# Kernel optimization log

Hardware: AMD Instinct MI355X
Metric: run time of the kernel (lower is better)

## Reference

```python
import jax, jax.numpy as jnp
import numpy as np

BS, HID, INP, SPAN, OUT, DAYS = 32768, 128, 64, 8, 2, 20


def _init(key, shape, fan_in):
    # mimic torch default uniform(-1/sqrt(fan), 1/sqrt(fan)) init
    bound = 1.0 / np.sqrt(fan_in)
    return jax.random.uniform(key, shape, jnp.float32, -bound, bound)


def setup_inputs() -> dict:
    key = jax.random.key(0)
    ks = jax.random.split(key, 11)
    return {
        "hx": jax.random.normal(ks[0], (BS, HID), jnp.float32),
        # GRUCell params (PyTorch layout: gates stacked [r, z, n])
        "w_ih": _init(ks[1], (3 * HID, INP), HID),
        "w_hh": _init(ks[2], (3 * HID, HID), HID),
        "b_ih": _init(ks[3], (3 * HID,), HID),
        "b_hh": _init(ks[4], (3 * HID,), HID),
        # fc_in: hid -> input
        "fc_in_w": _init(ks[5], (INP, HID), HID),
        "fc_in_b": _init(ks[6], (INP,), HID),
        # fc_out: hid -> out
        "fc_out_w": _init(ks[7], (OUT, HID), HID),
        "fc_out_b": _init(ks[8], (OUT,), HID),
        # num_span_layer: hid -> num_span_classes
        "span_w": _init(ks[9], (SPAN, HID), HID),
        "span_b": _init(ks[10], (SPAN,), HID),
    }


def _gru_cell(x, h, w_ih, w_hh, b_ih, b_hh):
    gi = x @ w_ih.T + b_ih  # [B, 3H]
    gh = h @ w_hh.T + b_hh  # [B, 3H]
    i_r, i_z, i_n = jnp.split(gi, 3, axis=-1)
    h_r, h_z, h_n = jnp.split(gh, 3, axis=-1)
    r = jax.nn.sigmoid(i_r + h_r)
    z = jax.nn.sigmoid(i_z + h_z)
    n = jnp.tanh(i_n + r * h_n)
    return (1.0 - z) * n + z * h


def reference(hx, w_ih, w_hh, b_ih, b_hh, fc_in_w, fc_in_b,
              fc_out_w, fc_out_b, span_w, span_b):
    num_spans = jax.nn.softmax(hx @ span_w.T + span_b, axis=-1)  # [B, SPAN]
    x0 = jnp.zeros((hx.shape[0], fc_in_w.shape[0]), hx.dtype)  # zero first input

    def step(carry, _):
        h, x = carry
        h = _gru_cell(x, h, w_ih, w_hh, b_ih, b_hh)
        x = jax.nn.relu(h @ fc_in_w.T + fc_in_b)
        out = jax.nn.softmax(h @ fc_out_w.T + fc_out_b, axis=-1)  # [B, OUT]
        return (h, x), out

    _, outs = jax.lax.scan(step, (hx, x0), None, length=DAYS)  # [DAYS, B, OUT]
    outputs = jnp.transpose(outs, (1, 0, 2))  # [B, DAYS, OUT]
    return num_spans, outputs
```

## Files before the change

### kernel.cpp

```cpp
#include <hip/hip_runtime.h>
#include <hip/hip_bf16.h>

#define HID 128
#define INP 64
#define SPANN 8
#define NOUT 2
#define DAYS 20
#define RT 4
#define ROWS (16*RT)
#define NTH 512

typedef __attribute__((ext_vector_type(8))) short short8;
typedef __attribute__((ext_vector_type(4))) float f32x4;
typedef __attribute__((ext_vector_type(2))) float f32x2;
typedef unsigned int u32;
typedef __attribute__((ext_vector_type(2))) u32 u32x2;
typedef unsigned short u16;

#define MFMA(a,b,c) __builtin_amdgcn_mfma_f32_16x16x32_bf16(a,b,c,0,0,0)
#define RCPF(x)  __builtin_amdgcn_rcpf(x)
#define EXP2F(x) __builtin_amdgcn_exp2f(x)
#define LOG2E   1.4426950408889634f
#define NLOG2E  (-1.4426950408889634f)
#define LOG2E2  2.8853900817779268f

__device__ __forceinline__ u32 pack2(float a, float b){
    __hip_bfloat162 h = __float22bfloat162_rn(float2{a, b});
    u32 r; __builtin_memcpy(&r, &h, 4); return r;
}
__device__ __forceinline__ float asF(u32 u){ union{u32 u; float f;} v; v.u = u; return v.f; }
__device__ __forceinline__ float sig2(float a){ return RCPF(1.0f + EXP2F(a)); }
__device__ __forceinline__ float tanh2(float a){ return fmaf(-2.0f, RCPF(1.0f + EXP2F(a)), 1.0f); }

union frag_u { short8 s; u32 w[4]; };
__device__ __forceinline__ short8 ldfrag(const float* p, float sc){
    const f32x4 a = *(const f32x4*)p;
    const f32x4 b = *(const f32x4*)(p+4);
    frag_u f;
    f.w[0] = pack2(sc*a[0],sc*a[1]); f.w[1] = pack2(sc*a[2],sc*a[3]);
    f.w[2] = pack2(sc*b[0],sc*b[1]); f.w[3] = pack2(sc*b[2],sc*b[3]);
    return f.s;
}


__global__ __launch_bounds__(NTH, 2) void gru_mfma(
    const float* __restrict__ hx, const float* __restrict__ w_ih,
    const float* __restrict__ w_hh, const float* __restrict__ b_ih,
    const float* __restrict__ b_hh, const float* __restrict__ fc_in_w,
    const float* __restrict__ fc_in_b, const float* __restrict__ fc_out_w,
    const float* __restrict__ fc_out_b, const float* __restrict__ span_w,
    const float* __restrict__ span_b, float* __restrict__ out, int bs)
{
    __shared__ u16 hL[2][RT*2048];
    __shared__ u16 xL[RT*1024];
    __shared__ u16 finL[4*4*64*8];
    __shared__ float diffP[ROWS][9];

    const int tid = threadIdx.x;
    const int wid = tid >> 6;
    const int l   = tid & 63;
    const int r15 = l & 15;
    const int hi  = l >> 4;
    const int row0 = blockIdx.x * ROWS;
    const int mB  = wid & 3;
    const int rtB_off = wid >> 2;

    short8 whhR[4], whhZ[4], whhN[4];
    short8 wihR[2], wihZ[2], wihN[2];
    const int g0 = wid*16 + r15;
    #pragma unroll
    for (int ks = 0; ks < 4; ++ks){
        whhR[ks] = ldfrag(w_hh + (size_t)(      g0)*HID + ks*32 + hi*8, NLOG2E);
        whhZ[ks] = ldfrag(w_hh + (size_t)(128 + g0)*HID + ks*32 + hi*8, NLOG2E);
        whhN[ks] = ldfrag(w_hh + (size_t)(256 + g0)*HID + ks*32 + hi*8, LOG2E2);
    }
    #pragma unroll
    for (int ks = 0; ks < 2; ++ks){
        wihR[ks] = ldfrag(w_ih + (size_t)(      g0)*INP + ks*32 + hi*8, NLOG2E);
        wihZ[ks] = ldfrag(w_ih + (size_t)(128 + g0)*INP + ks*32 + hi*8, NLOG2E);
        wihN[ks] = ldfrag(w_ih + (size_t)(256 + g0)*INP + ks*32 + hi*8, LOG2E2);
    }

    for (int s = tid; s < 1024; s += NTH) {
        const int mt = s >> 8, ks = (s >> 6) & 3, ll = s & 63;
        short8 f = ldfrag(fc_in_w + (size_t)(mt*16 + (ll&15))*HID + ks*32 + (ll>>4)*8, 1.0f);
        *((short8*)finL + s) = f;
    }

    f32x4 bRv, bZv, bNiv, bNhv, fbv, wd4;
    const int c0 = wid*16 + hi*4;
    #pragma unroll
    for (int q = 0; q < 4; ++q){
        const int g = c0 + q;
        bRv[q]  = NLOG2E*(b_ih[g]       + b_hh[g]);
        bZv[q]  = NLOG2E*(b_ih[128 + g] + b_hh[128 + g]);
        bNiv[q] = LOG2E2* b_ih[256 + g];
        bNhv[q] = LOG2E2* b_hh[256 + g];
        fbv[q]  = fc_in_b[mB*16 + hi*4 + q];
        wd4[q]  = NLOG2E*(fc_out_w[g] - fc_out_w[HID + g]);
    }
    const float bd = NLOG2E*(fc_out_b[0] - fc_out_b[1]);

    const int wu32  = (wid>>1)*256 + (((wid&1)*2 + (hi>>1))*16 + r15)*4 + (hi&1)*2;
    const int xwu32 = (mB >>1)*256 + (((mB &1)*2 + (hi>>1))*16 + r15)*4 + (hi&1)*2;

    {
        #pragma unroll
        for (int rt = 0; rt < RT; ++rt){
            const f32x4 h4 = *(const f32x4*)(hx + (size_t)(row0 + rt*16 + r15)*HID + c0);
            u32x2 wv; wv[0] = pack2(h4[0], h4[1]); wv[1] = pack2(h4[2], h4[3]);
            *(u32x2*)((u32*)&hL[0][rt*2048] + wu32) = wv;
        }
        u32* xb = (u32*)&xL[0];
        for (int i = tid; i < RT*512; i += NTH) xb[i] = 0u;
    }
    __syncthreads();

    if (wid < 4){
        const short8 zz = {0,0,0,0,0,0,0,0};
        short8 spw[4];
        #pragma unroll
        for (int ks = 0; ks < 4; ++ks)
            spw[ks] = (r15 < SPANN) ? ldfrag(span_w + (size_t)r15*HID + ks*32 + hi*8, 1.0f) : zz;
        f32x4 acc = {0.f,0.f,0.f,0.f};
        #pragma unroll
        for (int q = 0; q < 4; ++q) if (hi < 2) acc[q] = span_b[hi*4 + q];
        const short8* hf = (const short8*)&hL[0][wid*2048];
        #pragma unroll
        for (int ks = 0; ks < 4; ++ks) acc = MFMA(spw[ks], hf[ks*64 + l], acc);
        if (hi < 2){
            float m = fmaxf(fmaxf(acc[0], acc[1]), fmaxf(acc[2], acc[3]));
            m = fmaxf(m, __shfl_xor(m, 16));
            float e0 = EXP2F(LOG2E*(acc[0]-m)), e1 = EXP2F(LOG2E*(acc[1]-m));
            float e2 = EXP2F(LOG2E*(acc[2]-m)), e3 = EXP2F(LOG2E*(acc[3]-m));
            float s = e0 + e1 + e2 + e3;
            s += __shfl_xor(s, 16);
            const float inv = RCPF(s);
            f32x4 o = {e0*inv, e1*inv, e2*inv, e3*inv};
            *(f32x4*)(out + (size_t)(row0 + wid*16 + r15)*SPANN + hi*4) = o;
        }
    }

    float* __restrict__ outp = out + (size_t)bs * SPANN;

    #define TILE_A(RTG, hRd_, hWr_) do { \
        const short8* hf = (const short8*)((hRd_) + (RTG)*2048); \
        const short8* xf = (const short8*)(xL + (RTG)*1024); \
        const short8 h0=hf[l], h1=hf[64+l], h2=hf[128+l], h3=hf[192+l]; \
        const short8 x0=xf[l], x1=xf[64+l]; \
        const u32x2 ho = *(const u32x2*)((const u32*)(hRd_) + (RTG)*1024 + wu32); \
        f32x4 aR  = MFMA(whhR[0], h0, bRv); \
        f32x4 aZ  = MFMA(whhZ[0], h0, bZv); \
        f32x4 aNh = MFMA(whhN[0], h0, bNhv); \
        aR = MFMA(whhR[1],h1,aR); aZ = MFMA(whhZ[1],h1,aZ); aNh = MFMA(whhN[1],h1,aNh); \
        aR = MFMA(whhR[2],h2,aR); aZ = MFMA(whhZ[2],h2,aZ); aNh = MFMA(whhN[2],h2,aNh); \
        aR = MFMA(whhR[3],h3,aR); aZ = MFMA(whhZ[3],h3,aZ); aNh = MFMA(whhN[3],h3,aNh); \
        f32x4 aNi = MFMA(wihN[0], x0, bNiv); \
        aR = MFMA(wihR[0],x0,aR); aZ = MFMA(wihZ[0],x0,aZ); \
        aNi = MFMA(wihN[1],x1,aNi); \
        aR = MFMA(wihR[1],x1,aR); aZ = MFMA(wihZ[1],x1,aZ); \
        const float hold[4] = { asF(ho[0]<<16), asF(ho[0]&0xFFFF0000u), \
                                asF(ho[1]<<16), asF(ho[1]&0xFFFF0000u) }; \
        float hn[4]; \
        _Pragma("unroll") for (int q=0;q<4;++q){ \
            const float rg = sig2(aR[q]); const float zg = sig2(aZ[q]); \
            const float nn = tanh2(fmaf(rg, aNh[q], aNi[q])); \
            hn[q] = fmaf(zg, hold[q]-nn, nn); } \
        u32x2 wv; wv[0]=pack2(hn[0],hn[1]); wv[1]=pack2(hn[2],hn[3]); \
        *(u32x2*)((hWr_) + (RTG)*1024 + wu32) = wv; \
        float pd = hn[0]*wd4[0]; pd = fmaf(hn[1],wd4[1],pd); \
        pd = fmaf(hn[2],wd4[2],pd); pd = fmaf(hn[3],wd4[3],pd); \
        pd += __shfl_xor(pd, 16); pd += __shfl_xor(pd, 32); \
        if (hi == 0) diffP[(RTG)*16 + r15][wid] = pd; \
    } while(0)

    #define OUT_STORE(d_, gb_) do { \
        if (wid == 7 && l < 32) { \
            const int rowIdx = (gb_)*32 + l; \
            const float* dp = &diffP[rowIdx][0]; \
            const float s = ((dp[0]+dp[1])+(dp[2]+dp[3])) + ((dp[4]+dp[5])+(dp[6]+dp[7])); \
            const float p0 = sig2(s + bd); \
            f32x2 o = {p0, 1.0f - p0}; \
            *(f32x2*)(outp + ((size_t)(row0 + rowIdx)*DAYS + (d_))*NOUT) = o; \
        } \
    } while(0)

    #define TILE_B(d_, gb_, hSrc) do { \
        if ((d_) < DAYS-1) { \
            const int rtB = 2*(gb_) + rtB_off; \
            const short8* hf = (const short8*)((hSrc) + rtB*2048); \
            const short8 h0=hf[l], h1=hf[64+l], h2=hf[128+l], h3=hf[192+l]; \
            const short8* fp = (const short8*)finL + mB*256 + l; \
            f32x4 ax = MFMA(fp[0],   h0, fbv); \
            ax       = MFMA(fp[64],  h1, ax); \
            ax       = MFMA(fp[128], h2, ax); \
            ax       = MFMA(fp[192], h3, ax); \
            u32x2 wv; \
            wv[0] = pack2(fmaxf(ax[0],0.f), fmaxf(ax[1],0.f)); \
            wv[1] = pack2(fmaxf(ax[2],0.f), fmaxf(ax[3],0.f)); \
            *(u32x2*)((u32*)xL + rtB*512 + xwu32) = wv; \
        } \
        OUT_STORE(d_, gb_); \
    } while(0)

    #pragma unroll 1
    for (int d = 0; d < DAYS; ++d){
        const u16* hRd = hL[d & 1];
        u32*       hWr = (u32*)hL[(d & 1) ^ 1];

        TILE_A(0, hRd, hWr);
        TILE_A(1, hRd, hWr);
        if (d > 0) TILE_B(d-1, 1, hRd);
        __syncthreads();

        TILE_A(2, hRd, hWr);
        TILE_A(3, hRd, hWr);
        TILE_B(d, 0, (const u16*)hWr);
        __syncthreads();
    }
    OUT_STORE(DAYS-1, 1);

    #undef TILE_A
    #undef TILE_B
    #undef OUT_STORE
}

extern "C" void kernel_launch(void* const* d_in, const int* in_sizes, int n_in,
                              void* d_out, int out_size, void* d_ws, size_t ws_size,
                              hipStream_t stream) {
    const float* hx       = (const float*)d_in[0];
    const float* w_ih     = (const float*)d_in[1];
    const float* w_hh     = (const float*)d_in[2];
    const float* b_ih     = (const float*)d_in[3];
    const float* b_hh     = (const float*)d_in[4];
    const float* fc_in_w  = (const float*)d_in[5];
    const float* fc_in_b  = (const float*)d_in[6];
    const float* fc_out_w = (const float*)d_in[7];
    const float* fc_out_b = (const float*)d_in[8];
    const float* span_w   = (const float*)d_in[9];
    const float* span_b   = (const float*)d_in[10];
    float* out = (float*)d_out;

    const int bs = in_sizes[0] / HID;
    dim3 grid(bs / ROWS), block(NTH);
    gru_mfma<<<grid, block, 0, stream>>>(hx, w_ih, w_hh, b_ih, b_hh,
                                         fc_in_w, fc_in_b, fc_out_w, fc_out_b,
                                         span_w, span_b, out, bs);
}
```

Before: 143.3 us.

## Stagger GRU and fc_in tile order across waves, keep hidden state in registers

Odd waves now run the fc_in (TILE_B) matmul before their GRU tiles, while even waves keep the original order. This is meant to spread MFMA and LDS pressure between barriers. Each wave also keeps its previous hidden-state slice in fp32 registers instead of re-reading the bf16 copy from LDS, which drops one LDS load per tile and avoids bf16 rounding of the z*h term. MFMA blocks are wrapped in s_setprio, and the diffP reduction now uses padded, aligned vector reads. The cost is more live registers, which could hurt occupancy at two blocks of 512 threads.

```diff
diff --git a/kernel.cpp b/kernel.cpp
--- a/kernel.cpp
+++ b/kernel.cpp
@@ -28,7 +28,6 @@
     __hip_bfloat162 h = __float22bfloat162_rn(float2{a, b});
     u32 r; __builtin_memcpy(&r, &h, 4); return r;
 }
-__device__ __forceinline__ float asF(u32 u){ union{u32 u; float f;} v; v.u = u; return v.f; }
 __device__ __forceinline__ float sig2(float a){ return RCPF(1.0f + EXP2F(a)); }
 __device__ __forceinline__ float tanh2(float a){ return fmaf(-2.0f, RCPF(1.0f + EXP2F(a)), 1.0f); }
 
@@ -54,7 +53,7 @@
     __shared__ u16 hL[2][RT*2048];
     __shared__ u16 xL[RT*1024];
     __shared__ u16 finL[4*4*64*8];
-    __shared__ float diffP[ROWS][9];
+    __shared__ __attribute__((aligned(16))) float diffP[ROWS][12];
 
     const int tid = threadIdx.x;
     const int wid = tid >> 6;
@@ -104,13 +103,15 @@
     const int wu32  = (wid>>1)*256 + (((wid&1)*2 + (hi>>1))*16 + r15)*4 + (hi&1)*2;
     const int xwu32 = (mB >>1)*256 + (((mB &1)*2 + (hi>>1))*16 + r15)*4 + (hi&1)*2;
 
+    f32x4 hOld0, hOld1, hOld2, hOld3;
     {
-        #pragma unroll
-        for (int rt = 0; rt < RT; ++rt){
-            const f32x4 h4 = *(const f32x4*)(hx + (size_t)(row0 + rt*16 + r15)*HID + c0);
-            u32x2 wv; wv[0] = pack2(h4[0], h4[1]); wv[1] = pack2(h4[2], h4[3]);
-            *(u32x2*)((u32*)&hL[0][rt*2048] + wu32) = wv;
-        }
+        #define LOADH(RTG, HO) do { \
+            const f32x4 h4 = *(const f32x4*)(hx + (size_t)(row0 + (RTG)*16 + r15)*HID + c0); \
+            HO = h4; \
+            u32x2 wv; wv[0] = pack2(h4[0], h4[1]); wv[1] = pack2(h4[2], h4[3]); \
+            *(u32x2*)((u32*)&hL[0][(RTG)*2048] + wu32) = wv; } while(0)
+        LOADH(0, hOld0); LOADH(1, hOld1); LOADH(2, hOld2); LOADH(3, hOld3);
+        #undef LOADH
         u32* xb = (u32*)&xL[0];
         for (int i = tid; i < RT*512; i += NTH) xb[i] = 0u;
     }
@@ -143,12 +144,12 @@
 
     float* __restrict__ outp = out + (size_t)bs * SPANN;
 
-    #define TILE_A(RTG, hRd_, hWr_) do { \
+    #define TILE_A(RTG, hRd_, hWr_, HO) do { \
         const short8* hf = (const short8*)((hRd_) + (RTG)*2048); \
         const short8* xf = (const short8*)(xL + (RTG)*1024); \
         const short8 h0=hf[l], h1=hf[64+l], h2=hf[128+l], h3=hf[192+l]; \
         const short8 x0=xf[l], x1=xf[64+l]; \
-        const u32x2 ho = *(const u32x2*)((const u32*)(hRd_) + (RTG)*1024 + wu32); \
+        __builtin_amdgcn_s_setprio(1); \
         f32x4 aR  = MFMA(whhR[0], h0, bRv); \
         f32x4 aZ  = MFMA(whhZ[0], h0, bZv); \
         f32x4 aNh = MFMA(whhN[0], h0, bNhv); \
@@ -159,13 +160,12 @@
         aR = MFMA(wihR[0],x0,aR); aZ = MFMA(wihZ[0],x0,aZ); \
         aNi = MFMA(wihN[1],x1,aNi); \
         aR = MFMA(wihR[1],x1,aR); aZ = MFMA(wihZ[1],x1,aZ); \
-        const float hold[4] = { asF(ho[0]<<16), asF(ho[0]&0xFFFF0000u), \
-                                asF(ho[1]<<16), asF(ho[1]&0xFFFF0000u) }; \
+        __builtin_amdgcn_s_setprio(0); \
         float hn[4]; \
         _Pragma("unroll") for (int q=0;q<4;++q){ \
             const float rg = sig2(aR[q]); const float zg = sig2(aZ[q]); \
             const float nn = tanh2(fmaf(rg, aNh[q], aNi[q])); \
-            hn[q] = fmaf(zg, hold[q]-nn, nn); } \
+            hn[q] = fmaf(zg, HO[q]-nn, nn); HO[q] = hn[q]; } \
         u32x2 wv; wv[0]=pack2(hn[0],hn[1]); wv[1]=pack2(hn[2],hn[3]); \
         *(u32x2*)((hWr_) + (RTG)*1024 + wu32) = wv; \
         float pd = hn[0]*wd4[0]; pd = fmaf(hn[1],wd4[1],pd); \
@@ -177,8 +177,9 @@
     #define OUT_STORE(d_, gb_) do { \
         if (wid == 7 && l < 32) { \
             const int rowIdx = (gb_)*32 + l; \
-            const float* dp = &diffP[rowIdx][0]; \
-            const float s = ((dp[0]+dp[1])+(dp[2]+dp[3])) + ((dp[4]+dp[5])+(dp[6]+dp[7])); \
+            const f32x4 v0 = *(const f32x4*)&diffP[rowIdx][0]; \
+            const f32x4 v1 = *(const f32x4*)&diffP[rowIdx][4]; \
+            const float s = ((v0[0]+v0[1])+(v0[2]+v0[3])) + ((v1[0]+v1[1])+(v1[2]+v1[3])); \
             const float p0 = sig2(s + bd); \
             f32x2 o = {p0, 1.0f - p0}; \
             *(f32x2*)(outp + ((size_t)(row0 + rowIdx)*DAYS + (d_))*NOUT) = o; \
@@ -191,10 +192,12 @@
             const short8* hf = (const short8*)((hSrc) + rtB*2048); \
             const short8 h0=hf[l], h1=hf[64+l], h2=hf[128+l], h3=hf[192+l]; \
             const short8* fp = (const short8*)finL + mB*256 + l; \
+            __builtin_amdgcn_s_setprio(1); \
             f32x4 ax = MFMA(fp[0],   h0, fbv); \
             ax       = MFMA(fp[64],  h1, ax); \
             ax       = MFMA(fp[128], h2, ax); \
             ax       = MFMA(fp[192], h3, ax); \
+            __builtin_amdgcn_s_setprio(0); \
             u32x2 wv; \
             wv[0] = pack2(fmaxf(ax[0],0.f), fmaxf(ax[1],0.f)); \
             wv[1] = pack2(fmaxf(ax[2],0.f), fmaxf(ax[3],0.f)); \
@@ -208,14 +211,26 @@
         const u16* hRd = hL[d & 1];
         u32*       hWr = (u32*)hL[(d & 1) ^ 1];
 
-        TILE_A(0, hRd, hWr);
-        TILE_A(1, hRd, hWr);
-        if (d > 0) TILE_B(d-1, 1, hRd);
+        if (wid & 1) {
+            if (d > 0) TILE_B(d-1, 1, hRd);
+            TILE_A(0, hRd, hWr, hOld0);
+            TILE_A(1, hRd, hWr, hOld1);
+        } else {
+            TILE_A(0, hRd, hWr, hOld0);
+            TILE_A(1, hRd, hWr, hOld1);
+            if (d > 0) TILE_B(d-1, 1, hRd);
+        }
         __syncthreads();
 
-        TILE_A(2, hRd, hWr);
-        TILE_A(3, hRd, hWr);
-        TILE_B(d, 0, (const u16*)hWr);
+        if (wid & 1) {
+            TILE_B(d, 0, (const u16*)hWr);
+            TILE_A(2, hRd, hWr, hOld2);
+            TILE_A(3, hRd, hWr, hOld3);
+        } else {
+            TILE_A(2, hRd, hWr, hOld2);
+            TILE_A(3, hRd, hWr, hOld3);
+            TILE_B(d, 0, (const u16*)hWr);
+        }
         __syncthreads();
     }
     OUT_STORE(DAYS-1, 1);
```

Result: slower. 155.6 us (+8.6%).

## Switch GRU kernel to 32x32x16 MFMA with 128-row tiles

Applied to the files above, without the earlier changes.

Moves the GRU recurrence from 16x16x32 to 32x32x16 bf16 MFMA and doubles rows per block to 128, with a new LDS fragment layout for h, x and fc_in weights. Biases are injected via an extra MFMA against a ones column instead of accumulator init, and fc_in bias is folded in as a ninth k-slice. The previous software-pipelined overlap of the fc_in projection with the next tiles is replaced by a simpler two-phase schedule per day. This is meant to raise MFMA throughput per instruction and cut weight-fragment reuse overhead. In exchange it uses more registers and LDS and loses the earlier overlap.

```diff
diff --git a/kernel.cpp b/kernel.cpp
--- a/kernel.cpp
+++ b/kernel.cpp
@@ -6,18 +6,18 @@
 #define SPANN 8
 #define NOUT 2
 #define DAYS 20
-#define RT 4
-#define ROWS (16*RT)
+#define ROWS 128
 #define NTH 512
 
-typedef __attribute__((ext_vector_type(8))) short short8;
-typedef __attribute__((ext_vector_type(4))) float f32x4;
-typedef __attribute__((ext_vector_type(2))) float f32x2;
+typedef __attribute__((ext_vector_type(8)))  short short8;
+typedef __attribute__((ext_vector_type(16))) float f32x16;
+typedef __attribute__((ext_vector_type(4)))  float f32x4;
+typedef __attribute__((ext_vector_type(2)))  float f32x2;
 typedef unsigned int u32;
-typedef __attribute__((ext_vector_type(2))) u32 u32x2;
+typedef __attribute__((ext_vector_type(2)))  u32 u32x2;
 typedef unsigned short u16;
 
-#define MFMA(a,b,c) __builtin_amdgcn_mfma_f32_16x16x32_bf16(a,b,c,0,0,0)
+#define MFMA32(a,b,c) __builtin_amdgcn_mfma_f32_32x32x16_bf16(a,b,c,0,0,0)
 #define RCPF(x)  __builtin_amdgcn_rcpf(x)
 #define EXP2F(x) __builtin_amdgcn_exp2f(x)
 #define LOG2E   1.4426950408889634f
@@ -28,6 +28,7 @@
     __hip_bfloat162 h = __float22bfloat162_rn(float2{a, b});
     u32 r; __builtin_memcpy(&r, &h, 4); return r;
 }
+__device__ __forceinline__ u16 bf16u(float v){ return (u16)(pack2(v, v) & 0xFFFFu); }
 __device__ __forceinline__ float asF(u32 u){ union{u32 u; float f;} v; v.u = u; return v.f; }
 __device__ __forceinline__ float sig2(float a){ return RCPF(1.0f + EXP2F(a)); }
 __device__ __forceinline__ float tanh2(float a){ return fmaf(-2.0f, RCPF(1.0f + EXP2F(a)), 1.0f); }
@@ -43,7 +44,7 @@
 }
 
 
-__global__ __launch_bounds__(NTH, 2) void gru_mfma(
+__global__ __launch_bounds__(NTH, 2) void gru32(
     const float* __restrict__ hx, const float* __restrict__ w_ih,
     const float* __restrict__ w_hh, const float* __restrict__ b_ih,
     const float* __restrict__ b_hh, const float* __restrict__ fc_in_w,
@@ -51,178 +52,215 @@
     const float* __restrict__ fc_out_b, const float* __restrict__ span_w,
     const float* __restrict__ span_b, float* __restrict__ out, int bs)
 {
-    __shared__ u16 hL[2][RT*2048];
-    __shared__ u16 xL[RT*1024];
-    __shared__ u16 finL[4*4*64*8];
-    __shared__ float diffP[ROWS][9];
+    __shared__ __attribute__((aligned(16))) u16 hL[36864];
+    __shared__ __attribute__((aligned(16))) u16 xL[8192];
+    __shared__ __attribute__((aligned(16))) u16 finL[9216];
+    __shared__ u16 biasBL[512];
+    __shared__ float wdL[128];
+    __shared__ __attribute__((aligned(16))) float diffP[128][4];
 
     const int tid = threadIdx.x;
     const int wid = tid >> 6;
     const int l   = tid & 63;
-    const int r15 = l & 15;
-    const int hi  = l >> 4;
+    const int n31 = l & 31;
+    const int kg  = l >> 5;
     const int row0 = blockIdx.x * ROWS;
-    const int mB  = wid & 3;
-    const int rtB_off = wid >> 2;
-
-    short8 whhR[4], whhZ[4], whhN[4];
-    short8 wihR[2], wihZ[2], wihN[2];
-    const int g0 = wid*16 + r15;
+    const int ms  = wid & 3;
+    const int nt0 = wid >> 2;
+    const int msF = wid & 1;
+    const int ntF = wid >> 1;
+
+    short8 whhR[8], whhZ[8], whhN[8];
+    short8 wihR[4], wihZ[4], wihN[4];
+    {
+        const int mr = ms*32 + n31;
+        #pragma unroll
+        for (int ks = 0; ks < 8; ++ks){
+            whhR[ks] = ldfrag(w_hh + (size_t)(      mr)*HID + ks*16 + kg*8, NLOG2E);
+            whhZ[ks] = ldfrag(w_hh + (size_t)(128 + mr)*HID + ks*16 + kg*8, NLOG2E);
+            whhN[ks] = ldfrag(w_hh + (size_t)(256 + mr)*HID + ks*16 + kg*8, LOG2E2);
+        }
+        #pragma unroll
+        for (int ks = 0; ks < 4; ++ks){
+            wihR[ks] = ldfrag(w_ih + (size_t)(      mr)*INP + ks*16 + kg*8, NLOG2E);
+            wihZ[ks] = ldfrag(w_ih + (size_t)(128 + mr)*INP + ks*16 + kg*8, NLOG2E);
+            wihN[ks] = ldfrag(w_ih + (size_t)(256 + mr)*INP + ks*16 + kg*8, LOG2E2);
+        }
+    }
+    frag_u ob; ob.w[0] = (l < 32) ? 0x00003F80u : 0u; ob.w[1]=0; ob.w[2]=0; ob.w[3]=0;
+    const short8 onesB = ob.s;
+    const float bd = NLOG2E*(fc_out_b[0] - fc_out_b[1]);
+
     #pragma unroll
-    for (int ks = 0; ks < 4; ++ks){
-        whhR[ks] = ldfrag(w_hh + (size_t)(      g0)*HID + ks*32 + hi*8, NLOG2E);
-        whhZ[ks] = ldfrag(w_hh + (size_t)(128 + g0)*HID + ks*32 + hi*8, NLOG2E);
-        whhN[ks] = ldfrag(w_hh + (size_t)(256 + g0)*HID + ks*32 + hi*8, LOG2E2);
-    }
-    #pragma unroll
-    for (int ks = 0; ks < 2; ++ks){
-        wihR[ks] = ldfrag(w_ih + (size_t)(      g0)*INP + ks*32 + hi*8, NLOG2E);
-        wihZ[ks] = ldfrag(w_ih + (size_t)(128 + g0)*INP + ks*32 + hi*8, NLOG2E);
-        wihN[ks] = ldfrag(w_ih + (size_t)(256 + g0)*INP + ks*32 + hi*8, LOG2E2);
-    }
-
-    for (int s = tid; s < 1024; s += NTH) {
-        const int mt = s >> 8, ks = (s >> 6) & 3, ll = s & 63;
-        short8 f = ldfrag(fc_in_w + (size_t)(mt*16 + (ll&15))*HID + ks*32 + (ll>>4)*8, 1.0f);
-        *((short8*)finL + s) = f;
-    }
-
-    f32x4 bRv, bZv, bNiv, bNhv, fbv, wd4;
-    const int c0 = wid*16 + hi*4;
-    #pragma unroll
-    for (int q = 0; q < 4; ++q){
-        const int g = c0 + q;
-        bRv[q]  = NLOG2E*(b_ih[g]       + b_hh[g]);
-        bZv[q]  = NLOG2E*(b_ih[128 + g] + b_hh[128 + g]);
-        bNiv[q] = LOG2E2* b_ih[256 + g];
-        bNhv[q] = LOG2E2* b_hh[256 + g];
-        fbv[q]  = fc_in_b[mB*16 + hi*4 + q];
-        wd4[q]  = NLOG2E*(fc_out_w[g] - fc_out_w[HID + g]);
-    }
-    const float bd = NLOG2E*(fc_out_b[0] - fc_out_b[1]);
-
-    const int wu32  = (wid>>1)*256 + (((wid&1)*2 + (hi>>1))*16 + r15)*4 + (hi&1)*2;
-    const int xwu32 = (mB >>1)*256 + (((mB &1)*2 + (hi>>1))*16 + r15)*4 + (hi&1)*2;
-
-    {
-        #pragma unroll
-        for (int rt = 0; rt < RT; ++rt){
-            const f32x4 h4 = *(const f32x4*)(hx + (size_t)(row0 + rt*16 + r15)*HID + c0);
-            u32x2 wv; wv[0] = pack2(h4[0], h4[1]); wv[1] = pack2(h4[2], h4[3]);
-            *(u32x2*)((u32*)&hL[0][rt*2048] + wu32) = wv;
-        }
-        u32* xb = (u32*)&xL[0];
-        for (int i = tid; i < RT*512; i += NTH) xb[i] = 0u;
-    }
+    for (int i = 0; i < 8; ++i){
+        const int idx = tid + NTH*i;
+        const int row = idx >> 5, c4 = idx & 31;
+        const f32x4 v = ((const f32x4*)hx)[(size_t)(row0 + row)*32 + c4];
+        const int nt = row >> 5, nr = row & 31;
+        const int ks = c4 >> 2, kg2 = (c4 >> 1) & 1, jh = c4 & 1;
+        u32* p = (u32*)&hL[nt*4608 + ks*512 + (nr + 32*kg2)*8 + jh*4];
+        u32x2 wv; wv[0] = pack2(v[0], v[1]); wv[1] = pack2(v[2], v[3]);
+        *(u32x2*)p = wv;
+    }
+    for (int idx = tid; idx < 512; idx += NTH){
+        const int buf = idx >> 8, nt = (idx >> 6) & 3, l2 = idx & 63;
+        u32* p = (u32*)&hL[buf*18432 + nt*4608 + 8*512 + l2*8];
+        u32x2 a; a[0] = (l2 < 32) ? 0x00003F80u : 0u; a[1] = 0;
+        u32x2 z; z[0] = 0; z[1] = 0;
+        *(u32x2*)p = a; *((u32x2*)p + 1) = z;
+    }
+    for (int idx = tid; idx < 2048; idx += NTH){
+        u32x2 z; z[0] = 0; z[1] = 0; ((u32x2*)xL)[idx] = z;
+    }
+    for (int s = tid; s < 1152; s += NTH){
+        const int msf = (s >= 576) ? 1 : 0, r = s - msf*576;
+        const int ks = r >> 6, l2 = r & 63;
+        short8 f;
+        if (ks < 8){
+            f = ldfrag(fc_in_w + (size_t)(msf*32 + (l2&31))*HID + ks*16 + (l2>>5)*8, 1.0f);
+        } else {
+            frag_u u; u.w[0] = (l2 < 32) ? (u32)bf16u(fc_in_b[msf*32 + (l2&31)]) : 0u;
+            u.w[1]=0; u.w[2]=0; u.w[3]=0; f = u.s;
+        }
+        *((short8*)finL + msf*576 + ks*64 + l2) = f;
+    }
+    for (int idx = tid; idx < 512; idx += NTH){
+        const int g = idx >> 7, c = idx & 127;
+        float v;
+        if      (g == 0) v = NLOG2E*(b_ih[c]       + b_hh[c]);
+        else if (g == 1) v = NLOG2E*(b_ih[128 + c] + b_hh[128 + c]);
+        else if (g == 2) v = LOG2E2* b_hh[256 + c];
+        else             v = LOG2E2* b_ih[256 + c];
+        biasBL[idx] = bf16u(v);
+    }
+    if (tid < 128) wdL[tid] = NLOG2E*(fc_out_w[tid] - fc_out_w[128 + tid]);
     __syncthreads();
 
     if (wid < 4){
         const short8 zz = {0,0,0,0,0,0,0,0};
-        short8 spw[4];
-        #pragma unroll
-        for (int ks = 0; ks < 4; ++ks)
-            spw[ks] = (r15 < SPANN) ? ldfrag(span_w + (size_t)r15*HID + ks*32 + hi*8, 1.0f) : zz;
-        f32x4 acc = {0.f,0.f,0.f,0.f};
-        #pragma unroll
-        for (int q = 0; q < 4; ++q) if (hi < 2) acc[q] = span_b[hi*4 + q];
-        const short8* hf = (const short8*)&hL[0][wid*2048];
-        #pragma unroll
-        for (int ks = 0; ks < 4; ++ks) acc = MFMA(spw[ks], hf[ks*64 + l], acc);
-        if (hi < 2){
-            float m = fmaxf(fmaxf(acc[0], acc[1]), fmaxf(acc[2], acc[3]));
-            m = fmaxf(m, __shfl_xor(m, 16));
-            float e0 = EXP2F(LOG2E*(acc[0]-m)), e1 = EXP2F(LOG2E*(acc[1]-m));
-            float e2 = EXP2F(LOG2E*(acc[2]-m)), e3 = EXP2F(LOG2E*(acc[3]-m));
-            float s = e0 + e1 + e2 + e3;
-            s += __shfl_xor(s, 16);
-            const float inv = RCPF(s);
-            f32x4 o = {e0*inv, e1*inv, e2*inv, e3*inv};
-            *(f32x4*)(out + (size_t)(row0 + wid*16 + r15)*SPANN + hi*4) = o;
-        }
+        short8 spw[8];
+        #pragma unroll
+        for (int ks = 0; ks < 8; ++ks)
+            spw[ks] = (n31 < SPANN) ? ldfrag(span_w + (size_t)n31*HID + ks*16 + kg*8, 1.0f) : zz;
+        f32x16 acc = {0,0,0,0,0,0,0,0,0,0,0,0,0,0,0,0};
+        const short8* hb = (const short8*)&hL[wid*4608];
+        #pragma unroll
+        for (int ks = 0; ks < 8; ++ks) acc = MFMA32(spw[ks], hb[ks*64 + l], acc);
+        const f32x4 sb = *(const f32x4*)(span_b + kg*4);
+        const float s0 = acc[0]+sb[0], s1 = acc[1]+sb[1], s2 = acc[2]+sb[2], s3 = acc[3]+sb[3];
+        float m = fmaxf(fmaxf(s0, s1), fmaxf(s2, s3));
+        m = fmaxf(m, __shfl_xor(m, 32));
+        const float e0 = EXP2F(LOG2E*(s0-m)), e1 = EXP2F(LOG2E*(s1-m));
+        const float e2 = EXP2F(LOG2E*(s2-m)), e3 = EXP2F(LOG2E*(s3-m));
+        float sum = (e0+e1) + (e2+e3);
+        sum += __shfl_xor(sum, 32);
+        const float inv = RCPF(sum);
+        f32x4 o = {e0*inv, e1*inv, e2*inv, e3*inv};
+        *(f32x4*)(out + (size_t)(row0 + wid*32 + n31)*SPANN + kg*4) = o;
     }
 
     float* __restrict__ outp = out + (size_t)bs * SPANN;
-
-    #define TILE_A(RTG, hRd_, hWr_) do { \
-        const short8* hf = (const short8*)((hRd_) + (RTG)*2048); \
-        const short8* xf = (const short8*)(xL + (RTG)*1024); \
-        const short8 h0=hf[l], h1=hf[64+l], h2=hf[128+l], h3=hf[192+l]; \
-        const short8 x0=xf[l], x1=xf[64+l]; \
-        const u32x2 ho = *(const u32x2*)((const u32*)(hRd_) + (RTG)*1024 + wu32); \
-        f32x4 aR  = MFMA(whhR[0], h0, bRv); \
-        f32x4 aZ  = MFMA(whhZ[0], h0, bZv); \
-        f32x4 aNh = MFMA(whhN[0], h0, bNhv); \
-        aR = MFMA(whhR[1],h1,aR); aZ = MFMA(whhZ[1],h1,aZ); aNh = MFMA(whhN[1],h1,aNh); \
-        aR = MFMA(whhR[2],h2,aR); aZ = MFMA(whhZ[2],h2,aZ); aNh = MFMA(whhN[2],h2,aNh); \
-        aR = MFMA(whhR[3],h3,aR); aZ = MFMA(whhZ[3],h3,aZ); aNh = MFMA(whhN[3],h3,aNh); \
-        f32x4 aNi = MFMA(wihN[0], x0, bNiv); \
-        aR = MFMA(wihR[0],x0,aR); aZ = MFMA(wihZ[0],x0,aZ); \
-        aNi = MFMA(wihN[1],x1,aNi); \
-        aR = MFMA(wihR[1],x1,aR); aZ = MFMA(wihZ[1],x1,aZ); \
-        const float hold[4] = { asF(ho[0]<<16), asF(ho[0]&0xFFFF0000u), \
-                                asF(ho[1]<<16), asF(ho[1]&0xFFFF0000u) }; \
-        float hn[4]; \
-        _Pragma("unroll") for (int q=0;q<4;++q){ \
-            const float rg = sig2(aR[q]); const float zg = sig2(aZ[q]); \
-            const float nn = tanh2(fmaf(rg, aNh[q], aNi[q])); \
-            hn[q] = fmaf(zg, hold[q]-nn, nn); } \
-        u32x2 wv; wv[0]=pack2(hn[0],hn[1]); wv[1]=pack2(hn[2],hn[3]); \
-        *(u32x2*)((hWr_) + (RTG)*1024 + wu32) = wv; \
-        float pd = hn[0]*wd4[0]; pd = fmaf(hn[1],wd4[1],pd); \
-        pd = fmaf(hn[2],wd4[2],pd); pd = fmaf(hn[3],wd4[3],pd); \
-        pd += __shfl_xor(pd, 16); pd += __shfl_xor(pd, 32); \
-        if (hi == 0) diffP[(RTG)*16 + r15][wid] = pd; \
-    } while(0)
-
-    #define OUT_STORE(d_, gb_) do { \
-        if (wid == 7 && l < 32) { \
-            const int rowIdx = (gb_)*32 + l; \
-            const float* dp = &diffP[rowIdx][0]; \
-            const float s = ((dp[0]+dp[1])+(dp[2]+dp[3])) + ((dp[4]+dp[5])+(dp[6]+dp[7])); \
-            const float p0 = sig2(s + bd); \
-            f32x2 o = {p0, 1.0f - p0}; \
-            *(f32x2*)(outp + ((size_t)(row0 + rowIdx)*DAYS + (d_))*NOUT) = o; \
-        } \
-    } while(0)
-
-    #define TILE_B(d_, gb_, hSrc) do { \
-        if ((d_) < DAYS-1) { \
-            const int rtB = 2*(gb_) + rtB_off; \
-            const short8* hf = (const short8*)((hSrc) + rtB*2048); \
-            const short8 h0=hf[l], h1=hf[64+l], h2=hf[128+l], h3=hf[192+l]; \
-            const short8* fp = (const short8*)finL + mB*256 + l; \
-            f32x4 ax = MFMA(fp[0],   h0, fbv); \
-            ax       = MFMA(fp[64],  h1, ax); \
-            ax       = MFMA(fp[128], h2, ax); \
-            ax       = MFMA(fp[192], h3, ax); \
-            u32x2 wv; \
-            wv[0] = pack2(fmaxf(ax[0],0.f), fmaxf(ax[1],0.f)); \
-            wv[1] = pack2(fmaxf(ax[2],0.f), fmaxf(ax[3],0.f)); \
-            *(u32x2*)((u32*)xL + rtB*512 + xwu32) = wv; \
-        } \
-        OUT_STORE(d_, gb_); \
-    } while(0)
 
     #pragma unroll 1
     for (int d = 0; d < DAYS; ++d){
-        const u16* hRd = hL[d & 1];
-        u32*       hWr = (u32*)hL[(d & 1) ^ 1];
-
-        TILE_A(0, hRd, hWr);
-        TILE_A(1, hRd, hWr);
-        if (d > 0) TILE_B(d-1, 1, hRd);
+        const u16* hRd = hL + (d & 1)*18432;
+        u16*       hWr = hL + ((d & 1) ^ 1)*18432;
+
+        #pragma unroll
+        for (int t = 0; t < 2; ++t){
+            const int nt = nt0 + 2*t;
+            const short8* hb = (const short8*)(hRd + nt*4608);
+            const short8* xb = (const short8*)(xL  + nt*2048);
+
+            frag_u bR_, bZ_, bNh_, bNi_;
+            bR_.w[0]  = (l<32) ? (u32)biasBL[      ms*32 + n31] : 0u; bR_.w[1]=0;  bR_.w[2]=0;  bR_.w[3]=0;
+            bZ_.w[0]  = (l<32) ? (u32)biasBL[128 + ms*32 + n31] : 0u; bZ_.w[1]=0;  bZ_.w[2]=0;  bZ_.w[3]=0;
+            bNh_.w[0] = (l<32) ? (u32)biasBL[256 + ms*32 + n31] : 0u; bNh_.w[1]=0; bNh_.w[2]=0; bNh_.w[3]=0;
+            bNi_.w[0] = (l<32) ? (u32)biasBL[384 + ms*32 + n31] : 0u; bNi_.w[1]=0; bNi_.w[2]=0; bNi_.w[3]=0;
+
+            f32x16 aR  = {0,0,0,0,0,0,0,0,0,0,0,0,0,0,0,0};
+            f32x16 aZ  = {0,0,0,0,0,0,0,0,0,0,0,0,0,0,0,0};
+            f32x16 aNh = {0,0,0,0,0,0,0,0,0,0,0,0,0,0,0,0};
+            f32x16 aNi = {0,0,0,0,0,0,0,0,0,0,0,0,0,0,0,0};
+            aR  = MFMA32(bR_.s,  onesB, aR);
+            aZ  = MFMA32(bZ_.s,  onesB, aZ);
+            aNh = MFMA32(bNh_.s, onesB, aNh);
+            aNi = MFMA32(bNi_.s, onesB, aNi);
+            #pragma unroll
+            for (int ks = 0; ks < 8; ++ks){
+                const short8 hf = hb[ks*64 + l];
+                aR  = MFMA32(whhR[ks], hf, aR);
+                aZ  = MFMA32(whhZ[ks], hf, aZ);
+                aNh = MFMA32(whhN[ks], hf, aNh);
+            }
+            #pragma unroll
+            for (int ks = 0; ks < 4; ++ks){
+                const short8 xf = xb[ks*64 + l];
+                aR  = MFMA32(wihR[ks], xf, aR);
+                aZ  = MFMA32(wihZ[ks], xf, aZ);
+                aNi = MFMA32(wihN[ks], xf, aNi);
+            }
+
+            const u32* hoB = (const u32*)hRd + nt*2304 + ms*512 + n31*4 + 2*kg;
+            const u32x2 q0 = *(const u32x2*)(hoB      );
+            const u32x2 q1 = *(const u32x2*)(hoB + 128);
+            const u32x2 q2 = *(const u32x2*)(hoB + 256);
+            const u32x2 q3 = *(const u32x2*)(hoB + 384);
+            const u32 how[8] = {q0[0],q0[1],q1[0],q1[1],q2[0],q2[1],q3[0],q3[1]};
+
+            float hn[16];
+            #pragma unroll
+            for (int q = 0; q < 16; ++q){
+                const float hold = (q & 1) ? asF(how[q>>1] & 0xFFFF0000u)
+                                           : asF(how[q>>1] << 16);
+                const float rg = sig2(aR[q]);
+                const float zg = sig2(aZ[q]);
+                const float nn = tanh2(fmaf(rg, aNh[q], aNi[q]));
+                hn[q] = fmaf(zg, hold - nn, nn);
+            }
+            u32* hw = (u32*)hWr + nt*2304 + ms*512 + n31*4 + 2*kg;
+            { u32x2 wv; wv[0]=pack2(hn[0],hn[1]);   wv[1]=pack2(hn[2],hn[3]);   *(u32x2*)(hw      ) = wv; }
+            { u32x2 wv; wv[0]=pack2(hn[4],hn[5]);   wv[1]=pack2(hn[6],hn[7]);   *(u32x2*)(hw + 128) = wv; }
+            { u32x2 wv; wv[0]=pack2(hn[8],hn[9]);   wv[1]=pack2(hn[10],hn[11]); *(u32x2*)(hw + 256) = wv; }
+            { u32x2 wv; wv[0]=pack2(hn[12],hn[13]); wv[1]=pack2(hn[14],hn[15]); *(u32x2*)(hw + 384) = wv; }
+
+            const f32x4 w0 = *(const f32x4*)&wdL[ms*32      + 4*kg];
+            const f32x4 w1 = *(const f32x4*)&wdL[ms*32 + 8  + 4*kg];
+            const f32x4 w2 = *(const f32x4*)&wdL[ms*32 + 16 + 4*kg];
+            const f32x4 w3 = *(const f32x4*)&wdL[ms*32 + 24 + 4*kg];
+            float pd = hn[0]*w0[0];
+            pd = fmaf(hn[1],w0[1],pd);  pd = fmaf(hn[2],w0[2],pd);  pd = fmaf(hn[3],w0[3],pd);
+            pd = fmaf(hn[4],w1[0],pd);  pd = fmaf(hn[5],w1[1],pd);  pd = fmaf(hn[6],w1[2],pd);  pd = fmaf(hn[7],w1[3],pd);
+            pd = fmaf(hn[8],w2[0],pd);  pd = fmaf(hn[9],w2[1],pd);  pd = fmaf(hn[10],w2[2],pd); pd = fmaf(hn[11],w2[3],pd);
+            pd = fmaf(hn[12],w3[0],pd); pd = fmaf(hn[13],w3[1],pd); pd = fmaf(hn[14],w3[2],pd); pd = fmaf(hn[15],w3[3],pd);
+            pd += __shfl_xor(pd, 32);
+            if (l < 32) diffP[nt*32 + n31][ms] = pd;
+        }
         __syncthreads();
 
-        TILE_A(2, hRd, hWr);
-        TILE_A(3, hRd, hWr);
-        TILE_B(d, 0, (const u16*)hWr);
+        if (d < DAYS-1){
+            const short8* hb = (const short8*)(hWr + ntF*4608);
+            const short8* fp = (const short8*)finL + msF*576;
+            f32x16 ax = {0,0,0,0,0,0,0,0,0,0,0,0,0,0,0,0};
+            #pragma unroll
+            for (int ks = 0; ks < 9; ++ks)
+                ax = MFMA32(fp[ks*64 + l], hb[ks*64 + l], ax);
+            u32* xw = (u32*)xL + ntF*1024 + msF*512 + n31*4 + 2*kg;
+            { u32x2 wv; wv[0]=pack2(fmaxf(ax[0],0.f), fmaxf(ax[1],0.f));   wv[1]=pack2(fmaxf(ax[2],0.f), fmaxf(ax[3],0.f));   *(u32x2*)(xw      ) = wv; }
+            { u32x2 wv; wv[0]=pack2(fmaxf(ax[4],0.f), fmaxf(ax[5],0.f));   wv[1]=pack2(fmaxf(ax[6],0.f), fmaxf(ax[7],0.f));   *(u32x2*)(xw + 128) = wv; }
+            { u32x2 wv; wv[0]=pack2(fmaxf(ax[8],0.f), fmaxf(ax[9],0.f));   wv[1]=pack2(fmaxf(ax[10],0.f),fmaxf(ax[11],0.f));  *(u32x2*)(xw + 256) = wv; }
+            { u32x2 wv; wv[0]=pack2(fmaxf(ax[12],0.f),fmaxf(ax[13],0.f));  wv[1]=pack2(fmaxf(ax[14],0.f),fmaxf(ax[15],0.f));  *(u32x2*)(xw + 384) = wv; }
+        }
+        if (wid < 4 && l < 32){
+            const int row = wid*32 + l;
+            const f32x4 v = *(const f32x4*)&diffP[row][0];
+            const float s = (v[0] + v[1]) + (v[2] + v[3]);
+            const float p0 = sig2(s + bd);
+            f32x2 o = {p0, 1.0f - p0};
+            *(f32x2*)(outp + ((size_t)(row0 + row)*DAYS + d)*NOUT) = o;
+        }
         __syncthreads();
     }
-    OUT_STORE(DAYS-1, 1);
-
-    #undef TILE_A
-    #undef TILE_B
-    #undef OUT_STORE
 }
 
 extern "C" void kernel_launch(void* const* d_in, const int* in_sizes, int n_in,
@@ -243,7 +281,7 @@
 
     const int bs = in_sizes[0] / HID;
     dim3 grid(bs / ROWS), block(NTH);
-    gru_mfma<<<grid, block, 0, stream>>>(hx, w_ih, w_hh, b_ih, b_hh,
-                                         fc_in_w, fc_in_b, fc_out_w, fc_out_b,
-                                         span_w, span_b, out, bs);
-}
+    gru32<<<grid, block, 0, stream>>>(hx, w_ih, w_hh, b_ih, b_hh,
+                                      fc_in_w, fc_in_b, fc_out_w, fc_out_b,
+                                      span_w, span_b, out, bs);
+}
```

New measurement: 204.0 us. 1.42x slower.
